# Optimization experiments

Measured on AMD Instinct MI355X. Metric: run time of the kernel, lower is better.

## Reference

```python
import jax, jax.numpy as jnp
import numpy as np

N_NODES, N_EDGES = 10000, 160000
MUL0, MUL1 = 64, 32  # multiplicities of 0e and 1o in irreps_in
AVG_DEGREE = 16.0

# ---- real-basis Wigner 3j symbols (unit Frobenius norm, as in e3nn) ----
def _su2_gen(l):
    m = np.arange(-l, l + 1)
    Jz = np.diag(m).astype(complex)
    c = np.sqrt(l * (l + 1) - m[:-1] * (m[:-1] + 1))
    Jp = np.zeros((2 * l + 1, 2 * l + 1), complex)
    Jp[np.arange(1, 2 * l + 1), np.arange(2 * l)] = c
    Jm = Jp.conj().T
    return (Jp + Jm) / 2, (Jp - Jm) / 2j, Jz

def _c2r(l):
    U = np.zeros((2 * l + 1, 2 * l + 1), complex)
    s2 = 1 / np.sqrt(2)
    for m in range(-l, l + 1):
        if m > 0:
            U[l + m, l - m] = s2; U[l + m, l + m] = (-1) ** m * s2
        elif m == 0:
            U[l, l] = 1.0
        else:
            U[l + m, l + m] = 1j * s2; U[l + m, l - m] = -1j * (-1) ** m * s2
    return U

def _real_gen(l):
    U = _c2r(l)
    return [np.real(U @ (-1j * J) @ U.conj().T) for J in _su2_gen(l)]

def real_w3j(l1, l2, l3):
    A1, A2, A3 = _real_gen(l1), _real_gen(l2), _real_gen(l3)
    d1, d2, d3 = 2 * l1 + 1, 2 * l2 + 1, 2 * l3 + 1
    I1, I2, I3 = np.eye(d1), np.eye(d2), np.eye(d3)
    M = np.concatenate([
        np.kron(np.kron(A1[k], I2), I3) + np.kron(np.kron(I1, A2[k]), I3)
        + np.kron(np.kron(I1, I2), A3[k]) for k in range(3)], 0)
    v = np.linalg.svd(M)[2][-1]
    v = v / np.linalg.norm(v)
    nz = np.nonzero(np.abs(v) > 1e-8)[0][0]
    if v[nz] < 0:
        v = -v
    return jnp.asarray(v.reshape(d1, d2, d3), dtype=jnp.float32)

W000 = real_w3j(0, 0, 0); W011 = real_w3j(0, 1, 1); W022 = real_w3j(0, 2, 2)
W101 = real_w3j(1, 0, 1); W110 = real_w3j(1, 1, 0); W112 = real_w3j(1, 1, 2)
W121 = real_w3j(1, 2, 1)

# silu second-moment normalization constant (e3nn normalize2mom)
_x, _w = np.polynomial.hermite_e.hermegauss(128)
_s = _x / (1 + np.exp(-_x))
SILU_C = float(1.0 / np.sqrt((_w * _s ** 2).sum() / _w.sum()))
SQ3, SQ5 = float(np.sqrt(3.0)), float(np.sqrt(5.0))


def _forward(node_input, node_attr, edge_attr, edge_length_embedded,
             sc_w0, sc_w1, lin1_w0, lin1_w1, fc_w0, fc_w1,
             lin2_w0, lin2_w1, lin2_w2, edge_src, edge_dst):
    N = node_input.shape[0]
    E = edge_attr.shape[0]
    a = node_attr  # [N,1] scalar (0e) node attribute
    x0 = node_input[:, :MUL0]                       # [N,64]  0e block
    x1 = node_input[:, MUL0:].reshape(N, MUL1, 3)   # [N,32,3] 1o block

    # self connection sc = FullyConnectedTensorProduct(in, attr, out); no 2e path
    s0 = (x0 @ sc_w0) * a / jnp.sqrt(float(MUL0))
    s1 = jnp.einsum('nui,uv->nvi', x1, sc_w1) * a[:, :, None] / jnp.sqrt(float(MUL1))
    s = jnp.concatenate([s0, s1.reshape(N, -1),
                         jnp.zeros((N, 32 * 5), node_input.dtype)], 1)  # [N,320]

    # lin1 = FullyConnectedTensorProduct(in, attr, in)
    y0 = (x0 @ lin1_w0) * a / jnp.sqrt(float(MUL0))
    y1 = jnp.einsum('nui,uv->nvi', x1, lin1_w1) * a[:, :, None] / jnp.sqrt(float(MUL1))

    # radial FC net -> per-edge tensor-product weights [E,320]
    h = jax.nn.silu(edge_length_embedded @ fc_w0 / jnp.sqrt(8.0)) * SILU_C
    w = h @ fc_w1 / jnp.sqrt(64.0)

    xs0 = y0[edge_src][:, :, None]  # [E,64,1]
    xs1 = y1[edge_src]              # [E,32,3]
    e0, e1, e2 = edge_attr[:, :1], edge_attr[:, 1:4], edge_attr[:, 4:9]

    def path(x, e, wgt, C, pw):
        # x:[E,u,d1] e:[E,d2] wgt:[E,u] C:[d1,d2,d3] -> [E,u,d3]
        return pw * jnp.einsum('eui,ej,ijk,eu->euk', x, e, C, wgt)

    # 7 'uvu' instructions; weight slices in instruction order, outputs in sorted
    # irreps_mid order: 64x0e,32x0e,64x1o,32x1o,32x1o,64x2e,32x2e
    k0 = path(xs0, e0, w[:, 0:64],    W000, 1.0)   # 0e x 0e -> 0e, mul 64
    k2 = path(xs0, e1, w[:, 64:128],  W011, SQ3)   # 0e x 1o -> 1o, mul 64
    k5 = path(xs0, e2, w[:, 128:192], W022, SQ5)   # 0e x 2e -> 2e, mul 64
    k3 = path(xs1, e0, w[:, 192:224], W101, SQ3)   # 1o x 0e -> 1o, mul 32
    k1 = path(xs1, e1, w[:, 224:256], W110, 1.0)   # 1o x 1o -> 0e, mul 32
    k6 = path(xs1, e1, w[:, 256:288], W112, SQ5)   # 1o x 1o -> 2e, mul 32
    k4 = path(xs1, e2, w[:, 288:320], W121, SQ3)   # 1o x 2e -> 1o, mul 32
    edge_feat = jnp.concatenate(
        [k0.reshape(E, -1), k1.reshape(E, -1), k2.reshape(E, -1), k3.reshape(E, -1),
         k4.reshape(E, -1), k5.reshape(E, -1), k6.reshape(E, -1)], 1)  # [E,960]

    agg = jax.ops.segment_sum(edge_feat, edge_dst, num_segments=N) / jnp.sqrt(AVG_DEGREE)

    # lin2 = FullyConnectedTensorProduct(mid, attr, out); per-l fused matmuls
    m0 = agg[:, :96]                        # 0e muls 64+32
    m1 = agg[:, 96:480].reshape(N, 128, 3)  # 1o muls 64+32+32
    m2 = agg[:, 480:960].reshape(N, 96, 5)  # 2e muls 64+32
    o0 = (m0 @ lin2_w0) * a / jnp.sqrt(96.0)
    o1 = jnp.einsum('nui,uv->nvi', m1, lin2_w1) * a[:, :, None] / jnp.sqrt(128.0)
    o2 = jnp.einsum('nui,uv->nvi', m2, lin2_w2) * a[:, :, None] / jnp.sqrt(96.0)
    xo = jnp.concatenate([o0, o1.reshape(N, -1), o2.reshape(N, -1)], 1)  # [N,320]

    c_s = jnp.sin(jnp.pi / 8)
    c_x = jnp.cos(jnp.pi / 8)
    mask = jnp.concatenate([jnp.ones(160), jnp.zeros(160)]).astype(node_input.dtype)
    return c_s * s + (1.0 - mask + c_x * mask) * xo


def setup_inputs() -> dict:
    key = jax.random.key(0)
    ks = jax.random.split(key, 16)
    f = jax.random.normal
    return {
        'node_input': f(ks[0], (N_NODES, 160), jnp.float32),
        'node_attr': jnp.ones((N_NODES, 1), jnp.float32),
        'edge_src': jax.random.randint(ks[1], (N_EDGES,), 0, N_NODES, dtype=jnp.int32),
        'edge_dst': jax.random.randint(ks[2], (N_EDGES,), 0, N_NODES, dtype=jnp.int32),
        'edge_attr': f(ks[3], (N_EDGES, 9), jnp.float32),
        'edge_length_embedded': jax.random.uniform(ks[4], (N_EDGES, 8), dtype=jnp.float32),
        'sc_w0': f(ks[5], (64, 64), jnp.float32),
        'sc_w1': f(ks[6], (32, 32), jnp.float32),
        'lin1_w0': f(ks[7], (64, 64), jnp.float32),
        'lin1_w1': f(ks[8], (32, 32), jnp.float32),
        'fc_w0': f(ks[9], (8, 64), jnp.float32),
        'fc_w1': f(ks[10], (64, 320), jnp.float32),
        'lin2_w0': f(ks[11], (96, 64), jnp.float32),
        'lin2_w1': f(ks[12], (128, 32), jnp.float32),
        'lin2_w2': f(ks[13], (96, 32), jnp.float32),
    }


def reference(node_input, node_attr, edge_src, edge_dst, edge_attr, edge_length_embedded,
              sc_w0, sc_w1, lin1_w0, lin1_w1, fc_w0, fc_w1, lin2_w0, lin2_w1, lin2_w2):
    return _forward(node_input, node_attr, edge_attr, edge_length_embedded,
                    sc_w0, sc_w1, lin1_w0, lin1_w1, fc_w0, fc_w1,
                    lin2_w0, lin2_w1, lin2_w2, edge_src, edge_dst)
```

## Files before the change

### kernel.cpp

```cpp
#include <hip/hip_runtime.h>
#include <cstddef>
#include <cstdint>

#define N_NODES 10000
#define N_EDGES 160000

#define RS8    0.35355339059327373f
#define RS32   0.17677669529663687f
#define RS96   0.10206207261596575f
#define RS128  0.08838834764831845f
#define RS3    0.5773502691896258f
#define SQ3_   1.7320508075688772f
#define SQ5_   2.23606797749979f
#define A_     0.18257418583505536f
#define B_     0.31622776601683794f
#define SILU_C_ 1.6765208f
#define CS_    0.3826834323650898f
#define CX_    0.9238795325112867f
#define QDEG   0.25f

typedef __attribute__((ext_vector_type(8))) short bf16x8;
typedef __attribute__((ext_vector_type(4))) float f32x4;

__device__ inline float bf2f(unsigned v) {
  union { unsigned u; float f; } c; c.u = v << 16; return c.f;
}
__device__ inline float bfhi(unsigned v) {
  union { unsigned u; float f; } c; c.u = v & 0xffff0000u; return c.f;
}
__device__ inline unsigned short f2bf(float f) {
  union { float f; unsigned u; } c; c.f = f;
  unsigned r = c.u + 0x7fff + ((c.u >> 16) & 1);
  return (unsigned short)(r >> 16);
}
__device__ inline unsigned pack2bf(float a, float b) {
  return (unsigned)f2bf(a) | ((unsigned)f2bf(b) << 16);
}
__device__ inline float silu_c(float x) {
  return SILU_C_ * x / (1.f + __expf(-x));
}

__global__ __launch_bounds__(256) void k_prep(
    const int* __restrict__ edst, int* __restrict__ counts,
    const float* __restrict__ fc1, unsigned short* __restrict__ fc1p,
    const float* __restrict__ fc0, unsigned short* __restrict__ fc0p,
    const float* __restrict__ sc_w0, const float* __restrict__ sc_w1,
    const float* __restrict__ w0, const float* __restrict__ w1,
    const float* __restrict__ w2, const float* __restrict__ l1_w0,
    const float* __restrict__ l1_w1, unsigned short* __restrict__ Wp,
    unsigned short* __restrict__ Wyp) {
  int b = blockIdx.x, t = threadIdx.x;
  if (b < 625) {
    int e = b * 256 + t;
    if (e < N_EDGES) atomicAdd(&counts[edst[e]], 1);
    return;
  }
  if (b < 713) {
    int i = (b - 625) * 256 + t;
    if (i < 20480) {
      int j = i & 7, q = (i >> 3) & 3, n = (i >> 5) & 15, kq = (i >> 9) & 1, tt = i >> 10;
      int k = kq * 32 + q * 8 + j;
      fc1p[i] = f2bf(fc1[k * 320 + tt * 16 + n]);
    } else if (i < 22528) {
      int ii = i - 20480;
      int j = ii & 7;
      int lane = (ii >> 3) & 63;
      int ch = lane & 15, quad = lane >> 4;
      int nt = ii >> 9;
      int k = quad * 8 + j;
      float v = (k < 8) ? RS8 * fc0[k * 64 + nt * 16 + ch] : 0.f;
      fc0p[ii] = f2bf(v);
    }
    return;
  }
  int i = (b - 713) * 256 + t;
  if (i < 358400) {
    int j = i & 7;
    int lane = (i >> 3) & 63;
    int ch = lane & 15, quad = lane >> 4;
    int r = i >> 9;
    int nt = r / 35, ks = r - nt * 35;
    int k = ks * 32 + quad * 8 + j;
    int oc = nt * 16 + ch;
    float v = 0.f;
    if (k < 96) {
      if (oc < 64) v = (CX_ * RS96) * w0[k * 64 + oc];
    } else if (k < 480) {
      int tt = k - 96, u = tt / 3, ii = tt - u * 3;
      if (oc >= 64 && oc < 160) {
        int d = oc - 64, vv = d / 3, jj = d - vv * 3;
        if (jj == ii) v = (CX_ * RS128) * w1[u * 32 + vv];
      }
    } else if (k < 960) {
      int tt = k - 480, u = tt / 5, kk = tt - u * 5;
      if (oc >= 160) {
        int d = oc - 160, vv = d / 5, jj = d - vv * 5;
        if (jj == kk) v = RS96 * w2[u * 32 + vv];
      }
    } else if (k < 1024) {
      int u = k - 960;
      if (oc < 64) v = (CS_ * 0.125f) * sc_w0[u * 64 + oc];
    } else {
      int tt = k - 1024, u = tt / 3, ii = tt - u * 3;
      if (oc >= 64 && oc < 160) {
        int d = oc - 64, vv = d / 3, jj = d - vv * 3;
        if (jj == ii) v = (CS_ * RS32) * sc_w1[u * 32 + vv];
      }
    }
    Wp[i] = f2bf(v);
  } else if (i < 358400 + 30720) {
    int ii2 = i - 358400;
    int j = ii2 & 7;
    int lane = (ii2 >> 3) & 63;
    int ch = lane & 15, quad = lane >> 4;
    int r = ii2 >> 9;
    int nt = r / 5, ks = r - nt * 5;
    int k = ks * 32 + quad * 8 + j;
    int oc = nt * 16 + ch;
    float v = 0.f;
    if (k < 64) {
      if (oc < 64) v = 0.125f * l1_w0[k * 64 + oc];
    } else {
      int tt = k - 64, u = tt / 3, ci = tt - u * 3;
      if (oc >= 64) {
        int d = oc - 64, vv = d >> 2, jj = d & 3;
        if (jj == ci) v = RS32 * l1_w1[u * 32 + vv];
      }
    }
    Wyp[ii2] = f2bf(v);
  }
}

__global__ __launch_bounds__(256) void k_scan(const int* __restrict__ counts,
                                              int* __restrict__ offs,
                                              int* __restrict__ cur,
                                              int* __restrict__ dcur) {
  __shared__ int ps[256];
  __shared__ int dbin[256];
  int t = threadIdx.x;
  dbin[t] = 0;
  int base = t * 40;
  int sum = 0;
  for (int i = 0; i < 40; ++i) {
    int idx = base + i;
    if (idx < N_NODES) sum += counts[idx];
  }
  ps[t] = sum;
  __syncthreads();
  for (int off = 1; off < 256; off <<= 1) {
    int v = (t >= off) ? ps[t - off] : 0;
    __syncthreads();
    ps[t] += v;
    __syncthreads();
  }
  int run = (t == 0) ? 0 : ps[t - 1];
  for (int i = 0; i < 40; ++i) {
    int idx = base + i;
    if (idx < N_NODES) {
      int c = counts[idx];
      offs[idx] = run; cur[idx] = run;
      run += c;
      atomicAdd(&dbin[c < 255 ? c : 255], 1);
    }
  }
  __syncthreads();
  int rb = 255 - t;
  int v = dbin[rb];
  __syncthreads();
  ps[t] = v;
  __syncthreads();
  for (int off = 1; off < 256; off <<= 1) {
    int u = (t >= off) ? ps[t - off] : 0;
    __syncthreads();
    ps[t] += u;
    __syncthreads();
  }
  dcur[rb] = ps[t] - v;
}

__global__ __launch_bounds__(256) void k_perm(
    const int* __restrict__ edst, int* __restrict__ cur,
    const int* __restrict__ counts, const int* __restrict__ offs,
    int* __restrict__ dcur, int* __restrict__ order,
    int* __restrict__ obeg, int* __restrict__ ocnt,
    const float* __restrict__ ele, const float* __restrict__ eattr,
    const int* __restrict__ esrc, float* __restrict__ ed2a,
    float* __restrict__ ed2b) {
  __shared__ __align__(16) float sh_ea[256 * 9];
  __shared__ __align__(16) float sh_el[256 * 8];
  int t = threadIdx.x;
  int eb = blockIdx.x * 256;
  int e = eb + t;
  for (int i = t; i < 2304; i += 256) sh_ea[i] = eattr[(size_t)eb * 9 + i];
  {
    const float4* src = (const float4*)(ele + (size_t)eb * 8);
    float4* dst = (float4*)sh_el;
    dst[t] = src[t]; dst[t + 256] = src[t + 256];
  }
  __syncthreads();
  int d = edst[e];
  int p = atomicAdd(&cur[d], 1);
  const float* ea = sh_ea + t * 9;
  const float* el = sh_el + t * 8;
  float4 r0 = {ea[0], ea[1], ea[2], ea[3]};
  float4 r1 = {ea[4], ea[5], ea[6], ea[7]};
  float4 r2 = {ea[8], __int_as_float(esrc[e]), 0.f, 0.f};
  float4* da = (float4*)(ed2a + (size_t)p * 12);
  da[0] = r0; da[1] = r1; da[2] = r2;
  float4 r3 = {el[0], el[1], el[2], el[3]};
  float4 r4 = {el[4], el[5], el[6], el[7]};
  float4* db = (float4*)(ed2b + (size_t)p * 8);
  db[0] = r3; db[1] = r4;
  if (e < N_NODES) {
    int c = counts[e];
    int b = c < 255 ? c : 255;
    int q = atomicAdd(&dcur[b], 1);
    order[q] = e; obeg[q] = offs[e]; ocnt[q] = c;
  }
}

__device__ inline f32x4 wtile(const unsigned short* __restrict__ fc1p,
                              bf16x8 a0, bf16x8 a1, int mrow, int quad, int t) {
  f32x4 acc = {0.f, 0.f, 0.f, 0.f};
  bf16x8 b0 = *(const bf16x8*)(fc1p + ((size_t)((t * 2 + 0) * 16 + mrow) * 4 + quad) * 8);
  bf16x8 b1 = *(const bf16x8*)(fc1p + ((size_t)((t * 2 + 1) * 16 + mrow) * 4 + quad) * 8);
  acc = __builtin_amdgcn_mfma_f32_16x16x32_bf16(b0, a0, acc, 0, 0, 0);
  acc = __builtin_amdgcn_mfma_f32_16x16x32_bf16(b1, a1, acc, 0, 0, 0);
  return acc;
}

struct WgemmShared {
  __align__(16) unsigned short elb[64 * 32];
  __align__(16) unsigned short h[64 * 72];
};

__device__ void w_gemm_body(WgemmShared& sh, int blk,
    const float* __restrict__ ed2b, const unsigned short* __restrict__ fc0p,
    const unsigned short* __restrict__ fc1p, unsigned short* __restrict__ wout) {
  int t = threadIdx.x;
  int eb = blk * 64;
  {
    int e = t >> 2, q = t & 3;
    uint4 pk = {0u, 0u, 0u, 0u};
    if (q == 0) {
      const float4* ep = (const float4*)(ed2b + (size_t)(eb + e) * 8);
      float4 u = ep[0], v = ep[1];
      pk.x = pack2bf(u.x, u.y); pk.y = pack2bf(u.z, u.w);
      pk.z = pack2bf(v.x, v.y); pk.w = pack2bf(v.z, v.w);
    }
    *(uint4*)(sh.elb + e * 32 + q * 8) = pk;
  }
  __syncthreads();

  int wv = t >> 6, lane = t & 63;
  int ch16 = lane & 15, quad = lane >> 4;
  {
    bf16x8 af = *(const bf16x8*)(sh.elb + (wv * 16 + ch16) * 32 + quad * 8);
    bf16x8 b0 = *(const bf16x8*)(fc0p + 0 * 512 + lane * 8);
    bf16x8 b1 = *(const bf16x8*)(fc0p + 1 * 512 + lane * 8);
    bf16x8 b2 = *(const bf16x8*)(fc0p + 2 * 512 + lane * 8);
    bf16x8 b3 = *(const bf16x8*)(fc0p + 3 * 512 + lane * 8);
    f32x4 z = {0.f, 0.f, 0.f, 0.f};
    f32x4 h0 = __builtin_amdgcn_mfma_f32_16x16x32_bf16(b0, af, z, 0, 0, 0);
    f32x4 h1 = __builtin_amdgcn_mfma_f32_16x16x32_bf16(b1, af, z, 0, 0, 0);
    f32x4 h2 = __builtin_amdgcn_mfma_f32_16x16x32_bf16(b2, af, z, 0, 0, 0);
    f32x4 h3 = __builtin_amdgcn_mfma_f32_16x16x32_bf16(b3, af, z, 0, 0, 0);
    unsigned short* hb = sh.h + (wv * 16 + ch16) * 72 + quad * 4;
    uint2 s;
    s.x = pack2bf(silu_c(h0[0]), silu_c(h0[1]));
    s.y = pack2bf(silu_c(h0[2]), silu_c(h0[3]));
    *(uint2*)(hb + 0) = s;
    s.x = pack2bf(silu_c(h1[0]), silu_c(h1[1]));
    s.y = pack2bf(silu_c(h1[2]), silu_c(h1[3]));
    *(uint2*)(hb + 16) = s;
    s.x = pack2bf(silu_c(h2[0]), silu_c(h2[1]));
    s.y = pack2bf(silu_c(h2[2]), silu_c(h2[3]));
    *(uint2*)(hb + 32) = s;
    s.x = pack2bf(silu_c(h3[0]), silu_c(h3[1]));
    s.y = pack2bf(silu_c(h3[2]), silu_c(h3[3]));
    *(uint2*)(hb + 48) = s;
  }
  __syncthreads();

  int m0 = wv * 16;
  int mrow = lane & 15;
  bf16x8 a0 = *(const bf16x8*)(sh.h + (m0 + mrow) * 72 + quad * 8);
  bf16x8 a1 = *(const bf16x8*)(sh.h + (m0 + mrow) * 72 + 32 + quad * 8);
  char* wbase = (char*)wout + (size_t)(eb + m0 + mrow) * 640;
  const float K = 0.125f;
  #pragma unroll
  for (int tt = 0; tt < 4; ++tt) {
    f32x4 Av = wtile(fc1p, a0, a1, mrow, quad, tt);
    f32x4 Bv = wtile(fc1p, a0, a1, mrow, quad, tt + 4);
    uint4 st;
    st.x = pack2bf(Av[0] * K, Bv[0] * K);
    st.y = pack2bf(Av[1] * K, Bv[1] * K);
    st.z = pack2bf(Av[2] * K, Bv[2] * K);
    st.w = pack2bf(Av[3] * K, Bv[3] * K);
    *(uint4*)(wbase + 64 * tt + 16 * quad) = st;
  }
  #pragma unroll
  for (int tt = 8; tt < 12; ++tt) {
    f32x4 Cv = wtile(fc1p, a0, a1, mrow, quad, tt);
    uint2 st;
    st.x = pack2bf(Cv[0] * K, Cv[1] * K);
    st.y = pack2bf(Cv[2] * K, Cv[3] * K);
    *(uint2*)(wbase + 256 + 32 * (tt - 8) + 8 * quad) = st;
  }
  #pragma unroll
  for (int tt = 12; tt < 14; ++tt) {
    f32x4 Dv = wtile(fc1p, a0, a1, mrow, quad, tt);
    f32x4 Ev = wtile(fc1p, a0, a1, mrow, quad, tt + 2);
    f32x4 Fv = wtile(fc1p, a0, a1, mrow, quad, tt + 4);
    f32x4 Gv = wtile(fc1p, a0, a1, mrow, quad, tt + 6);
    char* db = wbase + 384 + 128 * (tt - 12) + 32 * quad;
    uint4 s0, s1;
    s0.x = pack2bf(Dv[0] * K, Ev[0] * K); s0.y = pack2bf(Fv[0] * K, Gv[0] * K);
    s0.z = pack2bf(Dv[1] * K, Ev[1] * K); s0.w = pack2bf(Fv[1] * K, Gv[1] * K);
    s1.x = pack2bf(Dv[2] * K, Ev[2] * K); s1.y = pack2bf(Fv[2] * K, Gv[2] * K);
    s1.z = pack2bf(Dv[3] * K, Ev[3] * K); s1.w = pack2bf(Fv[3] * K, Gv[3] * K);
    *(uint4*)(db) = s0;
    *(uint4*)(db + 16) = s1;
  }
}

#define YSTR 168
__device__ void npre_body(unsigned short* Ash, int blk,
    const float* __restrict__ xin, const float* __restrict__ attr,
    const unsigned short* __restrict__ Wyp, float* __restrict__ y) {
  int t = threadIdx.x;
  int nbase = blk * 16;
  for (int idx = t; idx < 16 * 80; idx += 256) {
    int row = idx / 80, c = idx - row * 80;
    const float* xp = xin + (size_t)(nbase + row) * 160 + 2 * c;
    *(unsigned*)(Ash + row * YSTR + 2 * c) = pack2bf(xp[0], xp[1]);
  }
  __syncthreads();
  int wid = t >> 6, lane = t & 63;
  int ch = lane & 15, quad = lane >> 4;
  const unsigned short* arow = Ash + ch * YSTR + quad * 8;
  f32x4 acc0 = {0.f,0.f,0.f,0.f}, acc1 = {0.f,0.f,0.f,0.f}, acc2 = {0.f,0.f,0.f,0.f};
  const unsigned short* wq0 = Wyp + ((size_t)(wid * 3 + 0) * 5 * 64 + lane) * 8;
  const unsigned short* wq1 = Wyp + ((size_t)(wid * 3 + 1) * 5 * 64 + lane) * 8;
  const unsigned short* wq2 = Wyp + ((size_t)(wid * 3 + 2) * 5 * 64 + lane) * 8;
  #pragma unroll
  for (int ks = 0; ks < 5; ++ks) {
    bf16x8 af  = *(const bf16x8*)(arow + ks * 32);
    bf16x8 w0f = *(const bf16x8*)(wq0 + ks * 512);
    bf16x8 w1f = *(const bf16x8*)(wq1 + ks * 512);
    bf16x8 w2f = *(const bf16x8*)(wq2 + ks * 512);
    acc0 = __builtin_amdgcn_mfma_f32_16x16x32_bf16(w0f, af, acc0, 0, 0, 0);
    acc1 = __builtin_amdgcn_mfma_f32_16x16x32_bf16(w1f, af, acc1, 0, 0, 0);
    acc2 = __builtin_amdgcn_mfma_f32_16x16x32_bf16(w2f, af, acc2, 0, 0, 0);
  }
  float a = attr[nbase + ch];
  float* yrow = y + (size_t)(nbase + ch) * 192 + quad * 4;
  { float4 st = {acc0[0]*a, acc0[1]*a, acc0[2]*a, acc0[3]*a};
    *(float4*)(yrow + (wid * 3 + 0) * 16) = st; }
  { float4 st = {acc1[0]*a, acc1[1]*a, acc1[2]*a, acc1[3]*a};
    *(float4*)(yrow + (wid * 3 + 1) * 16) = st; }
  { float4 st = {acc2[0]*a, acc2[1]*a, acc2[2]*a, acc2[3]*a};
    *(float4*)(yrow + (wid * 3 + 2) * 16) = st; }
}

__global__ __launch_bounds__(256) void k_midpre(
    const float* __restrict__ ed2b, const unsigned short* __restrict__ fc0p,
    const unsigned short* __restrict__ fc1p, unsigned short* __restrict__ wout,
    const float* __restrict__ xin, const float* __restrict__ attr,
    const unsigned short* __restrict__ Wyp, float* __restrict__ y) {
  __shared__ union ShU {
    WgemmShared w;
    unsigned short ash[16 * YSTR];
  } sh;
  if (blockIdx.x < 2500) {
    w_gemm_body(sh.w, blockIdx.x, ed2b, fc0p, fc1p, wout);
  } else {
    npre_body(sh.ash, blockIdx.x - 2500, xin, attr, Wyp, y);
  }
}

__global__ __launch_bounds__(256) void node_agg(
    const float* __restrict__ y, const float* __restrict__ ed2a,
    const unsigned short* __restrict__ wbuf,
    const int* __restrict__ order, const int* __restrict__ obeg,
    const int* __restrict__ ocnt, unsigned short* __restrict__ aggb) {
  int tid = threadIdx.x, wid = tid >> 6, lane = tid & 63, l31 = lane & 31;
  int gw = blockIdx.x * 4 + wid;
  int voY  = 4 * lane;
  int voX  = 256 + 16 * l31;
  int voAB = 4 * lane;
  int voC  = 256 + 2 * lane;
  int voDG = 384 + 8 * l31;

#define E_LOAD(S, idx)                                                         \
  if ((idx) < cnt) {                                                           \
    const float4* ep = (const float4*)(ed2a + (size_t)(beg + (idx)) * 12);     \
    PE0##S = ep[0]; PE1##S = ep[1]; PE2##S = ep[2];                            \
  }
#define V_LOAD(S, idx)                                                         \
  if ((idx) < cnt) {                                                           \
    int srcn = __float_as_int(PE2##S.y);                                       \
    const char* yb = (const char*)y + (size_t)srcn * 768;                      \
    Y##S = *(const float*)(yb + voY);                                          \
    X##S = *(const f32x4*)(yb + voX);                                          \
    const char* wb = (const char*)wbuf + (size_t)(beg + (idx)) * 640;          \
    AB##S = *(const unsigned*)(wb + voAB);                                     \
    Cw##S = *(const unsigned short*)(wb + voC);                                \
    DG##S = *(const uint2*)(wb + voDG);                                        \
  }
#define COMPUTE(S)                                                             \
  {                                                                            \
    float e0 = PE0##S.x, ey = PE0##S.y, ez = PE0##S.z, ex = PE0##S.w;          \
    float q0 = PE1##S.x, q1 = PE1##S.y, q2 = PE1##S.z, q3 = PE1##S.w;          \
    float q4 = PE2##S.x;                                                       \
    float Yv = Y##S, x0 = X##S.x, x1 = X##S.y, x2 = X##S.z;                    \
    float vA = bf2f(AB##S), vB = bfhi(AB##S), vC = bf2f(Cw##S);                \
    float vD = bf2f(DG##S.x), vE = bfhi(DG##S.x);                              \
    float vF = bf2f(DG##S.y), vG = bfhi(DG##S.y);                              \
    aK0 += Yv * e0 * vA;                                                       \
    float tB = Yv * vB; aK2x += tB * ey; aK2y += tB * ez; aK2z += tB * ex;     \
    float tC = Yv * vC;                                                        \
    aK5a += tC * q0; aK5b += tC * q1; aK5c += tC * q2;                         \
    aK5d += tC * q3; aK5e += tC * q4;                                          \
    float t1 = x0 * ey + x1 * ez + x2 * ex; aK1 += (RS3 * vE) * t1;            \
    float s3 = e0 * vD; aK3x += x0 * s3; aK3y += x1 * s3; aK3z += x2 * s3;     \
    float s4 = SQ3_ * vG;                                                      \
    aK4x += s4 * (B_ * (x2 * q0 + x1 * q1 - x0 * q4) - A_ * x0 * q2);          \
    aK4y += s4 * (B_ * (x0 * q1 + x2 * q3) + 2.f * A_ * x1 * q2);              \
    aK4z += s4 * (B_ * (x0 * q0 + x1 * q3 + x2 * q4) - A_ * x2 * q2);          \
    float s6 = SQ5_ * vF;                                                      \
    aK6a += s6 * (-B_ * (x0 * ex + x2 * ey));                                  \
    aK6b += s6 * (-B_ * (x0 * ez + x1 * ey));                                  \
    aK6c += s6 * ( A_ * (x0 * ey + x2 * ex - 2.f * x1 * ez));                  \
    aK6d += s6 * (-B_ * (x1 * ex + x2 * ez));                                  \
    aK6e += s6 * ( B_ * (x0 * ey - x2 * ex));                                  \
  }

  int n = order[gw], beg = obeg[gw], cnt = ocnt[gw];

  float aK0 = 0.f, aK2x = 0.f, aK2y = 0.f, aK2z = 0.f;
  float aK5a = 0.f, aK5b = 0.f, aK5c = 0.f, aK5d = 0.f, aK5e = 0.f;
  float aK1 = 0.f, aK3x = 0.f, aK3y = 0.f, aK3z = 0.f;
  float aK4x = 0.f, aK4y = 0.f, aK4z = 0.f;
  float aK6a = 0.f, aK6b = 0.f, aK6c = 0.f, aK6d = 0.f, aK6e = 0.f;

  float4 PE0a, PE1a, PE2a, PE0b, PE1b, PE2b;
  float Ya, Yb; f32x4 Xa, Xb;
  unsigned ABa, ABb; unsigned short Cwa, Cwb;
  uint2 DGa, DGb;

  E_LOAD(a, 0)
  E_LOAD(b, 1)
  V_LOAD(a, 0)

  int i = 0;
  while (i < cnt) {
    V_LOAD(b, i + 1)
    COMPUTE(a)
    E_LOAD(a, i + 2)
    ++i; if (i >= cnt) break;
    V_LOAD(a, i + 1)
    COMPUTE(b)
    E_LOAD(b, i + 2)
    ++i;
  }

  unsigned short* ag = aggb + (size_t)n * 960;
  ag[lane]           = f2bf(aK0  * QDEG);
  ag[96 + 3 * lane]  = f2bf(aK2x * QDEG);
  ag[97 + 3 * lane]  = f2bf(aK2y * QDEG);
  ag[98 + 3 * lane]  = f2bf(aK2z * QDEG);
  ag[480 + 5 * lane] = f2bf(aK5a * QDEG);
  ag[481 + 5 * lane] = f2bf(aK5b * QDEG);
  ag[482 + 5 * lane] = f2bf(aK5c * QDEG);
  ag[483 + 5 * lane] = f2bf(aK5d * QDEG);
  ag[484 + 5 * lane] = f2bf(aK5e * QDEG);
  if (lane < 32) {
    ag[64 + lane]      = f2bf(aK1  * QDEG);
    ag[288 + 3 * lane] = f2bf(aK3x * QDEG);
    ag[289 + 3 * lane] = f2bf(aK3y * QDEG);
    ag[290 + 3 * lane] = f2bf(aK3z * QDEG);
    ag[384 + 3 * lane] = f2bf(aK4x * QDEG);
    ag[385 + 3 * lane] = f2bf(aK4y * QDEG);
    ag[386 + 3 * lane] = f2bf(aK4z * QDEG);
    ag[800 + 5 * lane] = f2bf(aK6a * QDEG);
    ag[801 + 5 * lane] = f2bf(aK6b * QDEG);
    ag[802 + 5 * lane] = f2bf(aK6c * QDEG);
    ag[803 + 5 * lane] = f2bf(aK6d * QDEG);
    ag[804 + 5 * lane] = f2bf(aK6e * QDEG);
  }
#undef E_LOAD
#undef V_LOAD
#undef COMPUTE
}

#define ASTR 1128
__global__ __launch_bounds__(256) void k_out(
    const unsigned short* __restrict__ aggb, const float* __restrict__ xin,
    const float* __restrict__ attr, const unsigned short* __restrict__ Wp,
    float* __restrict__ out) {
  __shared__ __align__(16) unsigned short Ash[16 * ASTR];
  int t = threadIdx.x;
  int nbase = blockIdx.x * 16;
  for (int idx = t; idx < 16 * 480; idx += 256) {
    int row = idx / 480, c = idx - row * 480;
    *(unsigned*)(Ash + row * ASTR + 2 * c) =
        *(const unsigned*)(aggb + (size_t)(nbase + row) * 960 + 2 * c);
  }
  for (int idx = t; idx < 16 * 80; idx += 256) {
    int row = idx / 80, c = idx - row * 80;
    const float* xp = xin + (size_t)(nbase + row) * 160 + 2 * c;
    *(unsigned*)(Ash + row * ASTR + 960 + 2 * c) = pack2bf(xp[0], xp[1]);
  }
  __syncthreads();

  int wid = t >> 6, lane = t & 63;
  int ch = lane & 15, quad = lane >> 4;
  f32x4 acc0 = {0.f,0.f,0.f,0.f}, acc1 = {0.f,0.f,0.f,0.f};
  f32x4 acc2 = {0.f,0.f,0.f,0.f}, acc3 = {0.f,0.f,0.f,0.f};
  f32x4 acc4 = {0.f,0.f,0.f,0.f};
  const unsigned short* arow = Ash + ch * ASTR + quad * 8;
  const unsigned short* wq0 = Wp + ((size_t)(wid * 5 + 0) * 35 * 64 + lane) * 8;
  const unsigned short* wq1 = Wp + ((size_t)(wid * 5 + 1) * 35 * 64 + lane) * 8;
  const unsigned short* wq2 = Wp + ((size_t)(wid * 5 + 2) * 35 * 64 + lane) * 8;
  const unsigned short* wq3 = Wp + ((size_t)(wid * 5 + 3) * 35 * 64 + lane) * 8;
  const unsigned short* wq4 = Wp + ((size_t)(wid * 5 + 4) * 35 * 64 + lane) * 8;
  for (int ks = 0; ks < 35; ++ks) {
    bf16x8 af = *(const bf16x8*)(arow + ks * 32);
    bf16x8 w0f = *(const bf16x8*)(wq0 + ks * 512);
    bf16x8 w1f = *(const bf16x8*)(wq1 + ks * 512);
    bf16x8 w2f = *(const bf16x8*)(wq2 + ks * 512);
    bf16x8 w3f = *(const bf16x8*)(wq3 + ks * 512);
    bf16x8 w4f = *(const bf16x8*)(wq4 + ks * 512);
    acc0 = __builtin_amdgcn_mfma_f32_16x16x32_bf16(w0f, af, acc0, 0, 0, 0);
    acc1 = __builtin_amdgcn_mfma_f32_16x16x32_bf16(w1f, af, acc1, 0, 0, 0);
    acc2 = __builtin_amdgcn_mfma_f32_16x16x32_bf16(w2f, af, acc2, 0, 0, 0);
    acc3 = __builtin_amdgcn_mfma_f32_16x16x32_bf16(w3f, af, acc3, 0, 0, 0);
    acc4 = __builtin_amdgcn_mfma_f32_16x16x32_bf16(w4f, af, acc4, 0, 0, 0);
  }
  float a = attr[nbase + ch];
  float* orow = out + (size_t)(nbase + ch) * 320 + quad * 4;
  {
    float4 st = {acc0[0]*a, acc0[1]*a, acc0[2]*a, acc0[3]*a};
    *(float4*)(orow + (wid * 5 + 0) * 16) = st;
  }
  {
    float4 st = {acc1[0]*a, acc1[1]*a, acc1[2]*a, acc1[3]*a};
    *(float4*)(orow + (wid * 5 + 1) * 16) = st;
  }
  {
    float4 st = {acc2[0]*a, acc2[1]*a, acc2[2]*a, acc2[3]*a};
    *(float4*)(orow + (wid * 5 + 2) * 16) = st;
  }
  {
    float4 st = {acc3[0]*a, acc3[1]*a, acc3[2]*a, acc3[3]*a};
    *(float4*)(orow + (wid * 5 + 3) * 16) = st;
  }
  {
    float4 st = {acc4[0]*a, acc4[1]*a, acc4[2]*a, acc4[3]*a};
    *(float4*)(orow + (wid * 5 + 4) * 16) = st;
  }
}

extern "C" void kernel_launch(void* const* d_in, const int* in_sizes, int n_in,
                              void* d_out, int out_size, void* d_ws, size_t ws_size,
                              hipStream_t stream) {
  const float* node_input = (const float*)d_in[0];
  const float* node_attr  = (const float*)d_in[1];
  const int*   edge_src   = (const int*)d_in[2];
  const int*   edge_dst   = (const int*)d_in[3];
  const float* edge_attr  = (const float*)d_in[4];
  const float* ele        = (const float*)d_in[5];
  const float* sc_w0      = (const float*)d_in[6];
  const float* sc_w1      = (const float*)d_in[7];
  const float* l1_w0      = (const float*)d_in[8];
  const float* l1_w1      = (const float*)d_in[9];
  const float* fc_w0      = (const float*)d_in[10];
  const float* fc_w1      = (const float*)d_in[11];
  const float* l2_w0      = (const float*)d_in[12];
  const float* l2_w1      = (const float*)d_in[13];
  const float* l2_w2      = (const float*)d_in[14];
  float* out = (float*)d_out;

  char* base = (char*)d_ws;
  float* y              = (float*)(base);
  unsigned short* wbuf  = (unsigned short*)(base + 7680000);
  float* ed2a           = (float*)(base + 110080000);
  float* ed2b           = (float*)(base + 117760000);
  int* counts           = (int*)(base + 122880000);
  int* offs             = (int*)(base + 122920000);
  int* cur              = (int*)(base + 122960000);
  int* order            = (int*)(base + 123000000);
  int* obeg             = (int*)(base + 123040000);
  int* ocnt             = (int*)(base + 123080000);
  int* dcur             = (int*)(base + 123120000);
  unsigned short* fc1p  = (unsigned short*)(base + 123121024);
  unsigned short* aggb  = (unsigned short*)(base + 123162624);
  unsigned short* Wp    = (unsigned short*)(base + 142362624);
  unsigned short* Wyp   = (unsigned short*)(base + 143079424);
  unsigned short* fc0p  = (unsigned short*)(base + 143140864);

  hipMemsetAsync(counts, 0, N_NODES * sizeof(int), stream);
  hipLaunchKernelGGL(k_prep, dim3(2233), dim3(256), 0, stream,
                     edge_dst, counts, fc_w1, fc1p, fc_w0, fc0p,
                     sc_w0, sc_w1, l2_w0, l2_w1, l2_w2, l1_w0, l1_w1, Wp, Wyp);
  hipLaunchKernelGGL(k_scan, dim3(1), dim3(256), 0, stream, counts, offs, cur, dcur);
  hipLaunchKernelGGL(k_perm, dim3(N_EDGES / 256), dim3(256), 0, stream,
                     edge_dst, cur, counts, offs, dcur, order, obeg, ocnt,
                     ele, edge_attr, edge_src, ed2a, ed2b);
  hipLaunchKernelGGL(k_midpre, dim3(3125), dim3(256), 0, stream,
                     ed2b, fc0p, fc1p, wbuf, node_input, node_attr, Wyp, y);
  hipLaunchKernelGGL(node_agg, dim3(2500), dim3(256), 0, stream,
                     y, ed2a, wbuf, order, obeg, ocnt, aggb);
  hipLaunchKernelGGL(k_out, dim3(625), dim3(256), 0, stream,
                     aggb, node_input, node_attr, Wp, out);
}
```

Baseline: 198.2 us.

## Stage per-edge weight rows through double-buffered LDS chunks in node_agg

node_agg no longer reads each edge's 640-byte weight row with small scattered per-lane global loads. Each wave now loads 8-edge chunks with wide coalesced 16-byte loads into registers, writes them into a wave-private double-buffered LDS area, and reads the per-lane weights from LDS while the next chunk's global loads are in flight. The aim is better global load efficiency and overlap of weight fetches with compute. In exchange it uses 40 KB of LDS per block, which may limit occupancy, and it prefetches past each node's edge range, which wastes bandwidth on low-degree nodes and can read past the end of the buffer.

Result: slower. 221.7 us (+11.9%).

```diff
diff --git a/kernel.cpp b/kernel.cpp
--- a/kernel.cpp
+++ b/kernel.cpp
@@ -379,13 +379,16 @@
   }
 }
 
+#define NA_CB 5120
 __global__ __launch_bounds__(256) void node_agg(
     const float* __restrict__ y, const float* __restrict__ ed2a,
     const unsigned short* __restrict__ wbuf,
     const int* __restrict__ order, const int* __restrict__ obeg,
     const int* __restrict__ ocnt, unsigned short* __restrict__ aggb) {
+  __shared__ __align__(16) char wls[4][2 * NA_CB];
   int tid = threadIdx.x, wid = tid >> 6, lane = tid & 63, l31 = lane & 31;
   int gw = blockIdx.x * 4 + wid;
+  char* myw = &wls[wid][0];
   int voY  = 4 * lane;
   int voX  = 256 + 16 * l31;
   int voAB = 4 * lane;
@@ -397,13 +400,13 @@
     const float4* ep = (const float4*)(ed2a + (size_t)(beg + (idx)) * 12);     \
     PE0##S = ep[0]; PE1##S = ep[1]; PE2##S = ep[2];                            \
   }
-#define V_LOAD(S, idx)                                                         \
+#define V_LOADL(S, idx, LOFS)                                                  \
   if ((idx) < cnt) {                                                           \
     int srcn = __float_as_int(PE2##S.y);                                       \
     const char* yb = (const char*)y + (size_t)srcn * 768;                      \
     Y##S = *(const float*)(yb + voY);                                          \
     X##S = *(const f32x4*)(yb + voX);                                          \
-    const char* wb = (const char*)wbuf + (size_t)(beg + (idx)) * 640;          \
+    const char* wb = myw + (LOFS);                                             \
     AB##S = *(const unsigned*)(wb + voAB);                                     \
     Cw##S = *(const unsigned short*)(wb + voC);                                \
     DG##S = *(const uint2*)(wb + voDG);                                        \
@@ -435,6 +438,26 @@
     aK6d += s6 * (-B_ * (x1 * ex + x2 * ez));                                  \
     aK6e += s6 * ( B_ * (x0 * ey - x2 * ex));                                  \
   }
+#define CG(S, g) if ((g) < cnt) COMPUTE(S)
+#define W_ISSUE(c)                                                             \
+  {                                                                            \
+    const char* p = (const char*)wbuf +                                        \
+        ((size_t)beg + (size_t)(c) * 8) * 640 + lane * 16;                     \
+    sg0 = *(const uint4*)(p);                                                  \
+    sg1 = *(const uint4*)(p + 1024);                                           \
+    sg2 = *(const uint4*)(p + 2048);                                           \
+    sg3 = *(const uint4*)(p + 3072);                                           \
+    sg4 = *(const uint4*)(p + 4096);                                           \
+  }
+#define W_COMMIT(BOFS)                                                         \
+  {                                                                            \
+    char* q = myw + (BOFS) + lane * 16;                                        \
+    *(uint4*)(q)        = sg0;                                                 \
+    *(uint4*)(q + 1024) = sg1;                                                 \
+    *(uint4*)(q + 2048) = sg2;                                                 \
+    *(uint4*)(q + 3072) = sg3;                                                 \
+    *(uint4*)(q + 4096) = sg4;                                                 \
+  }
 
   int n = order[gw], beg = obeg[gw], cnt = ocnt[gw];
 
@@ -448,21 +471,30 @@
   float Ya, Yb; f32x4 Xa, Xb;
   unsigned ABa, ABb; unsigned short Cwa, Cwb;
   uint2 DGa, DGb;
-
+  uint4 sg0, sg1, sg2, sg3, sg4;
+
+  W_ISSUE(0)
+  W_COMMIT(0)
+  W_ISSUE(1)
   E_LOAD(a, 0)
   E_LOAD(b, 1)
-  V_LOAD(a, 0)
-
-  int i = 0;
-  while (i < cnt) {
-    V_LOAD(b, i + 1)
-    COMPUTE(a)
-    E_LOAD(a, i + 2)
-    ++i; if (i >= cnt) break;
-    V_LOAD(a, i + 1)
-    COMPUTE(b)
-    E_LOAD(b, i + 2)
-    ++i;
+  V_LOADL(a, 0, 0)
+
+  int nch = (cnt + 7) >> 3;
+  for (int c = 0; c < nch; ++c) {
+    int b0 = (c & 1) * NA_CB;
+    int b1 = NA_CB - b0;
+    W_COMMIT(b1)
+    W_ISSUE(c + 2)
+    int g0 = c * 8;
+    V_LOADL(b, g0 + 1, b0 + 640)  CG(a, g0)      E_LOAD(a, g0 + 2)
+    V_LOADL(a, g0 + 2, b0 + 1280) CG(b, g0 + 1)  E_LOAD(b, g0 + 3)
+    V_LOADL(b, g0 + 3, b0 + 1920) CG(a, g0 + 2)  E_LOAD(a, g0 + 4)
+    V_LOADL(a, g0 + 4, b0 + 2560) CG(b, g0 + 3)  E_LOAD(b, g0 + 5)
+    V_LOADL(b, g0 + 5, b0 + 3200) CG(a, g0 + 4)  E_LOAD(a, g0 + 6)
+    V_LOADL(a, g0 + 6, b0 + 3840) CG(b, g0 + 5)  E_LOAD(b, g0 + 7)
+    V_LOADL(b, g0 + 7, b0 + 4480) CG(a, g0 + 6)  E_LOAD(a, g0 + 8)
+    V_LOADL(a, g0 + 8, b1 + 0)    CG(b, g0 + 7)  E_LOAD(b, g0 + 9)
   }
 
   unsigned short* ag = aggb + (size_t)n * 960;
@@ -490,8 +522,11 @@
     ag[804 + 5 * lane] = f2bf(aK6e * QDEG);
   }
 #undef E_LOAD
-#undef V_LOAD
+#undef V_LOADL
 #undef COMPUTE
+#undef CG
+#undef W_ISSUE
+#undef W_COMMIT
 }
 
 #define ASTR 1128
```

## Recompute per-edge weights from hidden activations inside node aggregation

Applied to the files above, without the earlier changes.

The edge MLP's second GEMM moves out of the pre-pass and into node_agg. The pre-pass now writes only the 64-wide bf16 hidden vector per edge instead of the 320-wide weight row. Each wave recomputes 16 edges' weights at a time with MFMA into a shared-memory staging buffer before consuming them. The 0.125 scale is folded into the packed fc1 weights at prep time. This removes a large global write and read of edge weights, at the cost of extra MFMA work and shared memory in the aggregation kernel. It also assumes hbuf rows past cnt are readable, since the tile loads can run over the end of a node's edge list.

Result: slower. 272.4 us (+37.4%).

```diff
diff --git a/kernel.cpp b/kernel.cpp
--- a/kernel.cpp
+++ b/kernel.cpp
@@ -60,7 +60,7 @@
     if (i < 20480) {
       int j = i & 7, q = (i >> 3) & 3, n = (i >> 5) & 15, kq = (i >> 9) & 1, tt = i >> 10;
       int k = kq * 32 + q * 8 + j;
-      fc1p[i] = f2bf(fc1[k * 320 + tt * 16 + n]);
+      fc1p[i] = f2bf(0.125f * fc1[k * 320 + tt * 16 + n]);
     } else if (i < 22528) {
       int ii = i - 20480;
       int j = ii & 7;
@@ -236,7 +236,7 @@
 
 __device__ void w_gemm_body(WgemmShared& sh, int blk,
     const float* __restrict__ ed2b, const unsigned short* __restrict__ fc0p,
-    const unsigned short* __restrict__ fc1p, unsigned short* __restrict__ wout) {
+    unsigned short* __restrict__ hout) {
   int t = threadIdx.x;
   int eb = blk * 64;
   {
@@ -282,45 +282,10 @@
   }
   __syncthreads();
 
-  int m0 = wv * 16;
-  int mrow = lane & 15;
-  bf16x8 a0 = *(const bf16x8*)(sh.h + (m0 + mrow) * 72 + quad * 8);
-  bf16x8 a1 = *(const bf16x8*)(sh.h + (m0 + mrow) * 72 + 32 + quad * 8);
-  char* wbase = (char*)wout + (size_t)(eb + m0 + mrow) * 640;
-  const float K = 0.125f;
-  #pragma unroll
-  for (int tt = 0; tt < 4; ++tt) {
-    f32x4 Av = wtile(fc1p, a0, a1, mrow, quad, tt);
-    f32x4 Bv = wtile(fc1p, a0, a1, mrow, quad, tt + 4);
-    uint4 st;
-    st.x = pack2bf(Av[0] * K, Bv[0] * K);
-    st.y = pack2bf(Av[1] * K, Bv[1] * K);
-    st.z = pack2bf(Av[2] * K, Bv[2] * K);
-    st.w = pack2bf(Av[3] * K, Bv[3] * K);
-    *(uint4*)(wbase + 64 * tt + 16 * quad) = st;
-  }
-  #pragma unroll
-  for (int tt = 8; tt < 12; ++tt) {
-    f32x4 Cv = wtile(fc1p, a0, a1, mrow, quad, tt);
-    uint2 st;
-    st.x = pack2bf(Cv[0] * K, Cv[1] * K);
-    st.y = pack2bf(Cv[2] * K, Cv[3] * K);
-    *(uint2*)(wbase + 256 + 32 * (tt - 8) + 8 * quad) = st;
-  }
-  #pragma unroll
-  for (int tt = 12; tt < 14; ++tt) {
-    f32x4 Dv = wtile(fc1p, a0, a1, mrow, quad, tt);
-    f32x4 Ev = wtile(fc1p, a0, a1, mrow, quad, tt + 2);
-    f32x4 Fv = wtile(fc1p, a0, a1, mrow, quad, tt + 4);
-    f32x4 Gv = wtile(fc1p, a0, a1, mrow, quad, tt + 6);
-    char* db = wbase + 384 + 128 * (tt - 12) + 32 * quad;
-    uint4 s0, s1;
-    s0.x = pack2bf(Dv[0] * K, Ev[0] * K); s0.y = pack2bf(Fv[0] * K, Gv[0] * K);
-    s0.z = pack2bf(Dv[1] * K, Ev[1] * K); s0.w = pack2bf(Fv[1] * K, Gv[1] * K);
-    s1.x = pack2bf(Dv[2] * K, Ev[2] * K); s1.y = pack2bf(Fv[2] * K, Gv[2] * K);
-    s1.z = pack2bf(Dv[3] * K, Ev[3] * K); s1.w = pack2bf(Fv[3] * K, Gv[3] * K);
-    *(uint4*)(db) = s0;
-    *(uint4*)(db + 16) = s1;
+  for (int i = t; i < 2048; i += 256) {
+    int row = i >> 5, col = i & 31;
+    *(unsigned*)(hout + (size_t)(eb + row) * 64 + col * 2) =
+        *(const unsigned*)(sh.h + row * 72 + col * 2);
   }
 }
 
@@ -365,7 +330,7 @@
 
 __global__ __launch_bounds__(256) void k_midpre(
     const float* __restrict__ ed2b, const unsigned short* __restrict__ fc0p,
-    const unsigned short* __restrict__ fc1p, unsigned short* __restrict__ wout,
+    unsigned short* __restrict__ hout,
     const float* __restrict__ xin, const float* __restrict__ attr,
     const unsigned short* __restrict__ Wyp, float* __restrict__ y) {
   __shared__ union ShU {
@@ -373,19 +338,24 @@
     unsigned short ash[16 * YSTR];
   } sh;
   if (blockIdx.x < 2500) {
-    w_gemm_body(sh.w, blockIdx.x, ed2b, fc0p, fc1p, wout);
+    w_gemm_body(sh.w, blockIdx.x, ed2b, fc0p, hout);
   } else {
     npre_body(sh.ash, blockIdx.x - 2500, xin, attr, Wyp, y);
   }
 }
 
+#define EDST 656
 __global__ __launch_bounds__(256) void node_agg(
     const float* __restrict__ y, const float* __restrict__ ed2a,
-    const unsigned short* __restrict__ wbuf,
+    const unsigned short* __restrict__ hbuf,
+    const unsigned short* __restrict__ fc1p,
     const int* __restrict__ order, const int* __restrict__ obeg,
     const int* __restrict__ ocnt, unsigned short* __restrict__ aggb) {
+  __shared__ __align__(16) char wls[4][16 * EDST];
   int tid = threadIdx.x, wid = tid >> 6, lane = tid & 63, l31 = lane & 31;
   int gw = blockIdx.x * 4 + wid;
+  char* myw = &wls[wid][0];
+  int mrow = lane & 15, quad = lane >> 4;
   int voY  = 4 * lane;
   int voX  = 256 + 16 * l31;
   int voAB = 4 * lane;
@@ -397,13 +367,13 @@
     const float4* ep = (const float4*)(ed2a + (size_t)(beg + (idx)) * 12);     \
     PE0##S = ep[0]; PE1##S = ep[1]; PE2##S = ep[2];                            \
   }
-#define V_LOAD(S, idx)                                                         \
-  if ((idx) < cnt) {                                                           \
+#define V_LOADL(S, li)                                                         \
+  if ((li) < m) {                                                              \
     int srcn = __float_as_int(PE2##S.y);                                       \
     const char* yb = (const char*)y + (size_t)srcn * 768;                      \
     Y##S = *(const float*)(yb + voY);                                          \
     X##S = *(const f32x4*)(yb + voX);                                          \
-    const char* wb = (const char*)wbuf + (size_t)(beg + (idx)) * 640;          \
+    const char* wb = myw + (li) * EDST;                                        \
     AB##S = *(const unsigned*)(wb + voAB);                                     \
     Cw##S = *(const unsigned short*)(wb + voC);                                \
     DG##S = *(const uint2*)(wb + voDG);                                        \
@@ -449,20 +419,62 @@
   unsigned ABa, ABb; unsigned short Cwa, Cwb;
   uint2 DGa, DGb;
 
-  E_LOAD(a, 0)
-  E_LOAD(b, 1)
-  V_LOAD(a, 0)
-
-  int i = 0;
-  while (i < cnt) {
-    V_LOAD(b, i + 1)
-    COMPUTE(a)
-    E_LOAD(a, i + 2)
-    ++i; if (i >= cnt) break;
-    V_LOAD(a, i + 1)
-    COMPUTE(b)
-    E_LOAD(b, i + 2)
-    ++i;
+  for (int c0 = 0; c0 < cnt; c0 += 16) {
+    {
+      const unsigned short* hb = hbuf + (size_t)(beg + c0 + mrow) * 64;
+      bf16x8 a0 = *(const bf16x8*)(hb + quad * 8);
+      bf16x8 a1 = *(const bf16x8*)(hb + 32 + quad * 8);
+      char* wbase = myw + mrow * EDST;
+      #pragma unroll
+      for (int tt = 0; tt < 4; ++tt) {
+        f32x4 Av = wtile(fc1p, a0, a1, mrow, quad, tt);
+        f32x4 Bv = wtile(fc1p, a0, a1, mrow, quad, tt + 4);
+        uint4 st;
+        st.x = pack2bf(Av[0], Bv[0]);
+        st.y = pack2bf(Av[1], Bv[1]);
+        st.z = pack2bf(Av[2], Bv[2]);
+        st.w = pack2bf(Av[3], Bv[3]);
+        *(uint4*)(wbase + 64 * tt + 16 * quad) = st;
+      }
+      #pragma unroll
+      for (int tt = 8; tt < 12; ++tt) {
+        f32x4 Cv = wtile(fc1p, a0, a1, mrow, quad, tt);
+        uint2 st;
+        st.x = pack2bf(Cv[0], Cv[1]);
+        st.y = pack2bf(Cv[2], Cv[3]);
+        *(uint2*)(wbase + 256 + 32 * (tt - 8) + 8 * quad) = st;
+      }
+      #pragma unroll
+      for (int tt = 12; tt < 14; ++tt) {
+        f32x4 Dv = wtile(fc1p, a0, a1, mrow, quad, tt);
+        f32x4 Ev = wtile(fc1p, a0, a1, mrow, quad, tt + 2);
+        f32x4 Fv = wtile(fc1p, a0, a1, mrow, quad, tt + 4);
+        f32x4 Gv = wtile(fc1p, a0, a1, mrow, quad, tt + 6);
+        char* db = wbase + 384 + 128 * (tt - 12) + 32 * quad;
+        uint4 s0, s1;
+        s0.x = pack2bf(Dv[0], Ev[0]); s0.y = pack2bf(Fv[0], Gv[0]);
+        s0.z = pack2bf(Dv[1], Ev[1]); s0.w = pack2bf(Fv[1], Gv[1]);
+        s1.x = pack2bf(Dv[2], Ev[2]); s1.y = pack2bf(Fv[2], Gv[2]);
+        s1.z = pack2bf(Dv[3], Ev[3]); s1.w = pack2bf(Fv[3], Gv[3]);
+        *(uint4*)(db) = s0;
+        *(uint4*)(db + 16) = s1;
+      }
+    }
+    int m = cnt - c0; if (m > 16) m = 16;
+    E_LOAD(a, c0)
+    E_LOAD(b, c0 + 1)
+    V_LOADL(a, 0)
+    int i = 0;
+    while (i < m) {
+      V_LOADL(b, i + 1)
+      COMPUTE(a)
+      E_LOAD(a, c0 + i + 2)
+      ++i; if (i >= m) break;
+      V_LOADL(a, i + 1)
+      COMPUTE(b)
+      E_LOAD(b, c0 + i + 2)
+      ++i;
+    }
   }
 
   unsigned short* ag = aggb + (size_t)n * 960;
@@ -490,7 +502,7 @@
     ag[804 + 5 * lane] = f2bf(aK6e * QDEG);
   }
 #undef E_LOAD
-#undef V_LOAD
+#undef V_LOADL
 #undef COMPUTE
 }
 
@@ -584,7 +596,7 @@
 
   char* base = (char*)d_ws;
   float* y              = (float*)(base);
-  unsigned short* wbuf  = (unsigned short*)(base + 7680000);
+  unsigned short* hbuf  = (unsigned short*)(base + 7680000);
   float* ed2a           = (float*)(base + 110080000);
   float* ed2b           = (float*)(base + 117760000);
   int* counts           = (int*)(base + 122880000);
@@ -609,9 +621,9 @@
                      edge_dst, cur, counts, offs, dcur, order, obeg, ocnt,
                      ele, edge_attr, edge_src, ed2a, ed2b);
   hipLaunchKernelGGL(k_midpre, dim3(3125), dim3(256), 0, stream,
-                     ed2b, fc0p, fc1p, wbuf, node_input, node_attr, Wyp, y);
+                     ed2b, fc0p, hbuf, node_input, node_attr, Wyp, y);
   hipLaunchKernelGGL(node_agg, dim3(2500), dim3(256), 0, stream,
-                     y, ed2a, wbuf, order, obeg, ocnt, aggb);
+                     y, ed2a, hbuf, fc1p, order, obeg, ocnt, aggb);
   hipLaunchKernelGGL(k_out, dim3(625), dim3(256), 0, stream,
                      aggb, node_input, node_attr, Wp, out);
 }
```
